# Optimization experiments

Hardware: AMD Instinct MI355X
Metric: run time of the kernel (lower is better)

The kernel has to match this reference:

```python
import jax, jax.numpy as jnp
import numpy as np

EPS = 1e-8
NUM_ITER = 3
NUM_SLOTS = 8
NUM_HEADS = 4


def _ln(x, w, b):
    m = x.mean(-1, keepdims=True)
    v = x.var(-1, keepdims=True)
    return (x - m) / jnp.sqrt(v + 1e-5) * w + b


def setup_inputs() -> dict:
    key = jax.random.key(0)
    B, T, N, D, S, H = 16, 12, 1024, 256, 128, 256
    K = NUM_SLOTS
    ks = jax.random.split(key, 32)
    w = lambda i, shape: (0.02 * jax.random.normal(ks[i], shape)).astype(jnp.float32)
    f32 = jnp.float32
    return {
        'inputs': jax.random.normal(ks[0], (B, T, N, D), f32),
        'slots_noise': jax.random.normal(ks[1], (B, K, S), f32),
        'slot_mu': w(2, (1, 1, S)),
        'slot_log_sigma': w(3, (1, 1, S)),
        'ln_in_w': jnp.ones((D,), f32), 'ln_in_b': jnp.zeros((D,), f32),
        'ln_slots_w': jnp.ones((S,), f32), 'ln_slots_b': jnp.zeros((S,), f32),
        'ln_mlp_w': jnp.ones((S,), f32), 'ln_mlp_b': jnp.zeros((S,), f32),
        'Wq': w(4, (S, S)), 'Wk': w(5, (D, S)), 'Wv': w(6, (D, S)),
        'gru_Wih': w(7, (3 * S, S)), 'gru_Whh': w(8, (3 * S, S)),
        'gru_bih': jnp.zeros((3 * S,), f32), 'gru_bhh': jnp.zeros((3 * S,), f32),
        'mlp_W1': w(9, (S, H)), 'mlp_b1': jnp.zeros((H,), f32),
        'mlp_W2': w(10, (H, S)), 'mlp_b2': jnp.zeros((S,), f32),
        'p_ln1_w': jnp.ones((S,), f32), 'p_ln1_b': jnp.zeros((S,), f32),
        'p_Wq': w(11, (S, S)), 'p_Wk': w(12, (S, S)), 'p_Wv': w(13, (S, S)), 'p_Wo': w(14, (S, S)),
        'p_ln2_w': jnp.ones((S,), f32), 'p_ln2_b': jnp.zeros((S,), f32),
        'p_ffn_W1': w(15, (S, 4 * S)), 'p_ffn_b1': jnp.zeros((4 * S,), f32),
        'p_ffn_W2': w(16, (4 * S, S)), 'p_ffn_b2': jnp.zeros((S,), f32),
        'p_lnf_w': jnp.ones((S,), f32), 'p_lnf_b': jnp.zeros((S,), f32),
    }


def reference(inputs, slots_noise, slot_mu, slot_log_sigma,
              ln_in_w, ln_in_b, ln_slots_w, ln_slots_b, ln_mlp_w, ln_mlp_b,
              Wq, Wk, Wv, gru_Wih, gru_Whh, gru_bih, gru_bhh,
              mlp_W1, mlp_b1, mlp_W2, mlp_b2,
              p_ln1_w, p_ln1_b, p_Wq, p_Wk, p_Wv, p_Wo,
              p_ln2_w, p_ln2_b, p_ffn_W1, p_ffn_b1, p_ffn_W2, p_ffn_b2,
              p_lnf_w, p_lnf_b):
    B, T, N, D = inputs.shape
    S = slot_mu.shape[-1]
    K = NUM_SLOTS

    slots0 = slot_mu + jnp.exp(slot_log_sigma) * slots_noise  # (B,K,S)
    x = _ln(inputs, ln_in_w, ln_in_b)
    k = (x @ Wk) * (S ** -0.5)  # (B,T,N,S), pre-scaled keys
    v = x @ Wv                  # (B,T,N,S)

    def gru(u, h):  # torch GRUCell semantics; u,h: (B*K,S)
        gi = u @ gru_Wih.T + gru_bih
        gh = h @ gru_Whh.T + gru_bhh
        i_r, i_z, i_n = jnp.split(gi, 3, -1)
        h_r, h_z, h_n = jnp.split(gh, 3, -1)
        r = jax.nn.sigmoid(i_r + h_r)
        z = jax.nn.sigmoid(i_z + h_z)
        n = jnp.tanh(i_n + r * h_n)
        return (1.0 - z) * n + z * h

    def mha(y):  # (B,K,S) self-attention, pre-LN block style
        dh = S // NUM_HEADS
        split = lambda t: t.reshape(B, K, NUM_HEADS, dh).transpose(0, 2, 1, 3)
        q = split(y @ p_Wq) * (dh ** -0.5)
        kk = split(y @ p_Wk)
        vv = split(y @ p_Wv)
        a = jax.nn.softmax(jnp.einsum('bhqd,bhkd->bhqk', q, kk), -1)
        o = jnp.einsum('bhqk,bhkd->bhqd', a, vv).transpose(0, 2, 1, 3).reshape(B, K, S)
        return o @ p_Wo

    def predictor(s):
        s = s + mha(_ln(s, p_ln1_w, p_ln1_b))
        h = _ln(s, p_ln2_w, p_ln2_b)
        s = s + (jax.nn.relu(h @ p_ffn_W1 + p_ffn_b1) @ p_ffn_W2 + p_ffn_b2)
        return _ln(s, p_lnf_w, p_lnf_b)

    def step(slots, kv_t):
        k_t, v_t = kv_t  # (B,N,S) each
        attn_vis = None
        for i in range(NUM_ITER):
            slots_prev = slots
            q = _ln(slots, ln_slots_w, ln_slots_b) @ Wq          # (B,K,S)
            logits = jnp.einsum('bns,bks->bnk', k_t, q)           # (B,N,K)
            attn_vis = jax.nn.softmax(logits, -1)                 # over slots
            attn = attn_vis + EPS
            attn = attn / attn.sum(1, keepdims=True)              # normalize over inputs
            updates = jnp.einsum('bnk,bns->bks', attn, v_t)       # (B,K,S)
            slots = gru(updates.reshape(-1, S), slots_prev.reshape(-1, S)).reshape(B, K, S)
            if i < NUM_ITER - 1:
                h = _ln(slots, ln_mlp_w, ln_mlp_b)
                slots = slots + (jax.nn.relu(h @ mlp_W1 + mlp_b1) @ mlp_W2 + mlp_b2)
        return predictor(slots), (slots, attn_vis)

    kT = jnp.swapaxes(k, 0, 1)  # (T,B,N,S)
    vT = jnp.swapaxes(v, 0, 1)
    _, (slots_seq, attn_seq) = jax.lax.scan(step, slots0, (kT, vT))
    slots_collect = jnp.swapaxes(slots_seq, 0, 1)  # (B,T,K,S)
    attns_collect = jnp.swapaxes(attn_seq, 0, 1)   # (B,T,N,K)
    return slots_collect, attns_collect
```

## Files before the change

### kernel.cpp

```cpp
#include <hip/hip_runtime.h>
#include <hip/hip_bf16.h>

typedef _Float16 half8 __attribute__((ext_vector_type(8)));
typedef float floatx4 __attribute__((ext_vector_type(4)));

#define MFMA_F16(a, b, c) __builtin_amdgcn_mfma_f32_16x16x32_f16((a), (b), (c), 0, 0, 0)

__global__ void prep_w_kernel(const float* __restrict__ src, _Float16* __restrict__ dst,
                              int In, int Out, float scale, int doT) {
  int idx = blockIdx.x * 256 + threadIdx.x;
  if (idx >= In * Out) return;
  float v;
  if (doT) { int o = idx / In, i = idx - o * In; v = src[i * Out + o]; }
  else     { v = src[idx]; }
  dst[idx] = (_Float16)(v * scale);
}

__global__ void init_ctr_kernel(int* __restrict__ ctr) {
  if (threadIdx.x < 16) ctr[threadIdx.x] = 0;
}

__global__ __launch_bounds__(256) void gemm_kv_kernel(
    const float* __restrict__ x, const float* __restrict__ lnw_g,
    const float* __restrict__ lnb_g, const _Float16* __restrict__ WT,
    _Float16* __restrict__ kout, _Float16* __restrict__ vTout) {
  __shared__ union {
    struct { _Float16 A[128][72]; _Float16 B[128][72]; } s;
    _Float16 C[128][136];
  } u;
  __shared__ float s_mean[128], s_rstd[128], s_red[256][2], s_lnw[256], s_lnb[256];

  const int tid = threadIdx.x;
  const int bx = blockIdx.x, y = blockIdx.y;
  const size_t r0 = (size_t)bx * 128;
  const int w = tid >> 6, lane = tid & 63, quad = lane >> 4, l15 = lane & 15;

  s_lnw[tid] = lnw_g[tid];
  s_lnb[tid] = lnb_g[tid];
  {
    int row = tid >> 1, half = tid & 1;
    const float* p = x + (r0 + row) * 256 + half * 128;
    float s = 0.f, sq = 0.f;
    for (int i = 0; i < 32; i++) {
      float4 d = ((const float4*)p)[i];
      s += d.x + d.y + d.z + d.w;
      sq += d.x * d.x + d.y * d.y + d.z * d.z + d.w * d.w;
    }
    s_red[tid][0] = s; s_red[tid][1] = sq;
  }
  __syncthreads();
  if (tid < 128) {
    float s  = s_red[2 * tid][0] + s_red[2 * tid + 1][0];
    float sq = s_red[2 * tid][1] + s_red[2 * tid + 1][1];
    float m = s * (1.f / 256.f);
    float v = sq * (1.f / 256.f) - m * m;
    s_mean[tid] = m; s_rstd[tid] = rsqrtf(v + 1e-5f);
  }

  floatx4 acc[2][8];
  for (int rt = 0; rt < 2; rt++)
    for (int ct = 0; ct < 8; ct++) acc[rt][ct] = (floatx4){0.f, 0.f, 0.f, 0.f};

  for (int c = 0; c < 4; c++) {
    __syncthreads();
    for (int i = 0; i < 4; i++) {
      int g = tid + 256 * i;
      int row = g >> 3, c8 = g & 7;
      int col0 = c * 64 + c8 * 8;
      const float* p = x + (r0 + row) * 256 + col0;
      float4 d0 = ((const float4*)p)[0];
      float4 d1 = ((const float4*)p)[1];
      float f[8] = {d0.x, d0.y, d0.z, d0.w, d1.x, d1.y, d1.z, d1.w};
      float m = s_mean[row], rs = s_rstd[row];
      half8 hv;
      #pragma unroll
      for (int j = 0; j < 8; j++)
        hv[j] = (_Float16)((f[j] - m) * rs * s_lnw[col0 + j] + s_lnb[col0 + j]);
      *(half8*)&u.s.A[row][c8 * 8] = hv;
      *(half8*)&u.s.B[row][c8 * 8] = *(const half8*)(WT + (size_t)(y * 128 + row) * 256 + col0);
    }
    __syncthreads();
    #pragma unroll
    for (int ks = 0; ks < 2; ks++) {
      half8 af[2];
      af[0] = *(const half8*)&u.s.A[(2 * w) * 16 + l15][ks * 32 + quad * 8];
      af[1] = *(const half8*)&u.s.A[(2 * w + 1) * 16 + l15][ks * 32 + quad * 8];
      #pragma unroll
      for (int ct = 0; ct < 8; ct++) {
        half8 bf = *(const half8*)&u.s.B[ct * 16 + l15][ks * 32 + quad * 8];
        acc[0][ct] = MFMA_F16(af[0], bf, acc[0][ct]);
        acc[1][ct] = MFMA_F16(af[1], bf, acc[1][ct]);
      }
    }
  }

  const size_t bt = (size_t)(bx >> 3);
  const int n0loc = (bx & 7) * 128;
  if (y == 0) {
    for (int rt = 0; rt < 2; rt++)
      for (int ct = 0; ct < 8; ct++)
        #pragma unroll
        for (int r = 0; r < 4; r++) {
          size_t row = r0 + (2 * w + rt) * 16 + quad * 4 + r;
          kout[row * 128 + ct * 16 + l15] = (_Float16)acc[rt][ct][r];
        }
  } else {
    __syncthreads();
    for (int rt = 0; rt < 2; rt++)
      for (int ct = 0; ct < 8; ct++)
        #pragma unroll
        for (int r = 0; r < 4; r++)
          u.C[(2 * w + rt) * 16 + quad * 4 + r][ct * 16 + l15] = (_Float16)acc[rt][ct][r];
    __syncthreads();
    int s = tid >> 1, hf = tid & 1;
    for (int j = 0; j < 8; j++) {
      int nb = hf * 64 + j * 8;
      half8 tmp;
      #pragma unroll
      for (int e = 0; e < 8; e++) tmp[e] = u.C[nb + e][s];
      *(half8*)(vTout + (bt * 128 + s) * 1024 + n0loc + nb) = tmp;
    }
  }
}

struct P2Args {
  const _Float16 *kbuf, *vT;
  const _Float16 *WqT, *Wih, *Whh, *W1T, *W2T;
  const _Float16 *pQT, *pKT, *pVT, *pOT, *pF1T, *pF2T;
  const float *noise, *mu, *lsig;
  const float *lnsw, *lnsb, *lnmw, *lnmb;
  const float *bih, *bhh, *mb1, *mb2;
  const float *pl1w, *pl1b, *pl2w, *pl2b, *fb1, *fb2, *plfw, *plfb;
  float *out_slots, *out_attn;
  float *upd_p;
  float *col_p;
  float *vs_p;
  int   *ctr;
};

struct SH {
  _Float16 k_lds[128][136];
  _Float16 v_lds[128][136];
  float slots[8][128];
  _Float16 a16[16][136];
  _Float16 h16[16][136];
  union {
    struct { _Float16 qT[16][136]; _Float16 attnT[16][136]; } sa;
    struct { float gi[8][384]; float gh[8][384]; } gru;
    struct { _Float16 m16[16][264]; } mlp;
    struct { float qh[8][128]; float kh[8][128]; float vh[8][128]; float sc[4][8][8]; } mha;
    struct { _Float16 f16[16][520]; } ffn;
  } u;
  float colsum[8];
  float vsum[128];
  float bih[384], bhh[384], mb1[256], mb2[128], fb1[512], fb2[128];
  float lnsw[128], lnsb[128], lnmw[128], lnmb[128];
  float pl1w[128], pl1b[128], pl2w[128], pl2b[128], plfw[128], plfb[128];
};

__device__ __forceinline__ void group_barrier(int* ctr, int target) {
  __syncthreads();
  if (threadIdx.x == 0) {
    __hip_atomic_fetch_add(ctr, 1, __ATOMIC_ACQ_REL, __HIP_MEMORY_SCOPE_AGENT);
    while (__hip_atomic_load(ctr, __ATOMIC_ACQUIRE, __HIP_MEMORY_SCOPE_AGENT) < target)
      __builtin_amdgcn_s_sleep(1);
  }
  __syncthreads();
}

__device__ __forceinline__ void ln_to_a16(SH* sh, const float (*src)[128],
                                          const float* wv, const float* bv,
                                          int w, int lane) {
  if (w < 8) {
    float x0 = src[w][lane], x1 = src[w][lane + 64];
    float s = x0 + x1, sq = x0 * x0 + x1 * x1;
    #pragma unroll
    for (int m = 1; m < 64; m <<= 1) { s += __shfl_xor(s, m); sq += __shfl_xor(sq, m); }
    float mn = s * 0.0078125f;
    float vr = sq * 0.0078125f - mn * mn;
    float rs = rsqrtf(vr + 1e-5f);
    sh->a16[w][lane]      = (_Float16)((x0 - mn) * rs * wv[lane]      + bv[lane]);
    sh->a16[w][lane + 64] = (_Float16)((x1 - mn) * rs * wv[lane + 64] + bv[lane + 64]);
  } else {
    sh->a16[w][lane] = (_Float16)0.f;
    sh->a16[w][lane + 64] = (_Float16)0.f;
  }
}

__global__ __launch_bounds__(1024) void slot_attn_kernel(P2Args P) {
  __shared__ SH sh;
  const int tid = threadIdx.x;
  const int w = tid >> 6, lane = tid & 63, quad = lane >> 4, l15 = lane & 15;
  const int b = blockIdx.x & 15;
  const int g = blockIdx.x >> 4;
  const int n0 = g * 128;
  int* ctrb = P.ctr + b;
  int bar_phase = 0;

  for (int i = tid; i < 384; i += 1024) { sh.bih[i] = P.bih[i]; sh.bhh[i] = P.bhh[i]; }
  for (int i = tid; i < 256; i += 1024) sh.mb1[i] = P.mb1[i];
  for (int i = tid; i < 512; i += 1024) sh.fb1[i] = P.fb1[i];
  if (tid < 128) {
    sh.mb2[tid]  = P.mb2[tid];  sh.fb2[tid]  = P.fb2[tid];
    sh.lnsw[tid] = P.lnsw[tid]; sh.lnsb[tid] = P.lnsb[tid];
    sh.lnmw[tid] = P.lnmw[tid]; sh.lnmb[tid] = P.lnmb[tid];
    sh.pl1w[tid] = P.pl1w[tid]; sh.pl1b[tid] = P.pl1b[tid];
    sh.pl2w[tid] = P.pl2w[tid]; sh.pl2b[tid] = P.pl2b[tid];
    sh.plfw[tid] = P.plfw[tid]; sh.plfb[tid] = P.plfb[tid];
  }
  {
    int kk = tid >> 7, s = tid & 127;
    sh.slots[kk][s] = P.mu[s] + expf(P.lsig[s]) * P.noise[(b * 8 + kk) * 128 + s];
  }
  __syncthreads();

  for (int t = 0; t < 12; t++) {
    const _Float16* kt = P.kbuf + ((size_t)(b * 12 + t)) * 1024 * 128 + (size_t)n0 * 128;
    const _Float16* vt = P.vT   + ((size_t)(b * 12 + t)) * 128 * 1024 + n0;
    {
      int r = tid >> 4, c8 = (tid & 15) * 8;
      #pragma unroll
      for (int p = 0; p < 2; p++) {
        int row = p * 64 + r;
        *(half8*)&sh.k_lds[row][c8] = *(const half8*)(kt + (size_t)row * 128 + c8);
        *(half8*)&sh.v_lds[row][c8] = *(const half8*)(vt + (size_t)row * 1024 + c8);
      }
    }
    if (tid < 128) sh.vsum[tid] = 0.f;
    __syncthreads();
    {
      int s = tid >> 3, j = tid & 7;
      float a = 0.f;
      #pragma unroll
      for (int e = 0; e < 16; e++) a += (float)sh.v_lds[s][j * 16 + e];
      atomicAdd(&sh.vsum[s], a);
    }
    __syncthreads();
    if (tid < 128)
      __hip_atomic_store(&P.vs_p[(b * 8 + g) * 128 + tid], sh.vsum[tid],
                         __ATOMIC_RELAXED, __HIP_MEMORY_SCOPE_AGENT);

    for (int it = 0; it < 3; it++) {
      const int par = (t * 3 + it) & 1;
      float* updg = P.upd_p + ((size_t)(par * 16 + b) * 8 + g) * 1024;
      float* colg = P.col_p + ((size_t)(par * 16 + b) * 8 + g) * 8;
      if (w < 8) {
        float x0 = sh.slots[w][lane], x1 = sh.slots[w][lane + 64];
        sh.h16[w][lane] = (_Float16)x0; sh.h16[w][lane + 64] = (_Float16)x1;
        float s = x0 + x1, sq = x0 * x0 + x1 * x1;
        #pragma unroll
        for (int m = 1; m < 64; m <<= 1) { s += __shfl_xor(s, m); sq += __shfl_xor(sq, m); }
        float mn = s * 0.0078125f;
        float vr = sq * 0.0078125f - mn * mn;
        float rs = rsqrtf(vr + 1e-5f);
        sh.a16[w][lane]      = (_Float16)((x0 - mn) * rs * sh.lnsw[lane]      + sh.lnsb[lane]);
        sh.a16[w][lane + 64] = (_Float16)((x1 - mn) * rs * sh.lnsw[lane + 64] + sh.lnsb[lane + 64]);
      } else {
        sh.h16[w][lane] = (_Float16)0.f; sh.h16[w][lane + 64] = (_Float16)0.f;
        sh.a16[w][lane] = (_Float16)0.f; sh.a16[w][lane + 64] = (_Float16)0.f;
      }
      if (tid < 8) sh.colsum[tid] = 0.f;
      __syncthreads();
      if (w < 8) {
        floatx4 acc = (floatx4){0.f, 0.f, 0.f, 0.f};
        const _Float16* ar = &sh.a16[l15][quad * 8];
        const _Float16* br = P.WqT + (size_t)(w * 16 + l15) * 128 + quad * 8;
        #pragma unroll
        for (int ks = 0; ks < 4; ks++)
          acc = MFMA_F16(*(const half8*)(ar + ks * 32), *(const half8*)(br + ks * 32), acc);
        #pragma unroll
        for (int r = 0; r < 4; r++)
          sh.u.sa.qT[quad * 4 + r][w * 16 + l15] = (_Float16)acc[r];
      }
      __syncthreads();
      if (w < 8) {
        int nloc0 = w * 16;
        floatx4 acc = (floatx4){0.f, 0.f, 0.f, 0.f};
        const _Float16* ar = &sh.k_lds[nloc0 + l15][quad * 8];
        const _Float16* br = &sh.u.sa.qT[l15][quad * 8];
        #pragma unroll
        for (int ks = 0; ks < 4; ks++)
          acc = MFMA_F16(*(const half8*)(ar + ks * 32), *(const half8*)(br + ks * 32), acc);
        float cs = 0.f;
        #pragma unroll
        for (int r = 0; r < 4; r++) {
          float v = (l15 < 8) ? acc[r] : -3.0e38f;
          float mx = v;
          mx = fmaxf(mx, __shfl_xor(mx, 1, 16));
          mx = fmaxf(mx, __shfl_xor(mx, 2, 16));
          mx = fmaxf(mx, __shfl_xor(mx, 4, 16));
          mx = fmaxf(mx, __shfl_xor(mx, 8, 16));
          float pv = (l15 < 8) ? expf(v - mx) : 0.f;
          float ss = pv;
          ss += __shfl_xor(ss, 1, 16); ss += __shfl_xor(ss, 2, 16);
          ss += __shfl_xor(ss, 4, 16); ss += __shfl_xor(ss, 8, 16);
          float pn = pv / ss;
          cs += pn;
          int nloc = nloc0 + quad * 4 + r;
          sh.u.sa.attnT[l15][nloc] = (_Float16)pn;
          if (it == 2 && l15 < 8)
            P.out_attn[((size_t)(b * 12 + t) * 1024 + n0 + nloc) * 8 + l15] = pn;
        }
        cs += __shfl_xor(cs, 16); cs += __shfl_xor(cs, 32);
        if (lane < 8) atomicAdd(&sh.colsum[lane], cs);
      }
      __syncthreads();
      if (w < 8) {
        floatx4 acc = (floatx4){0.f, 0.f, 0.f, 0.f};
        const _Float16* ar = &sh.u.sa.attnT[l15][quad * 8];
        const _Float16* br = &sh.v_lds[w * 16 + l15][quad * 8];
        #pragma unroll
        for (int ks = 0; ks < 4; ks++)
          acc = MFMA_F16(*(const half8*)(ar + ks * 32), *(const half8*)(br + ks * 32), acc);
        int scol = w * 16 + l15;
        #pragma unroll
        for (int r = 0; r < 4; r++) {
          int slot = quad * 4 + r;
          if (slot < 8)
            __hip_atomic_store(&updg[slot * 128 + scol], acc[r],
                               __ATOMIC_RELAXED, __HIP_MEMORY_SCOPE_AGENT);
        }
      }
      if (tid < 8)
        __hip_atomic_store(&colg[tid], sh.colsum[tid],
                           __ATOMIC_RELAXED, __HIP_MEMORY_SCOPE_AGENT);
      bar_phase++;
      group_barrier(ctrb, 8 * bar_phase);
      {
        int slot = tid >> 7, scol = tid & 127;
        const float* up = P.upd_p + (size_t)(par * 16 + b) * 8 * 1024 + slot * 128 + scol;
        float sum = 0.f;
        #pragma unroll
        for (int gg = 0; gg < 8; gg++)
          sum += __hip_atomic_load((float*)(up + gg * 1024),
                                   __ATOMIC_RELAXED, __HIP_MEMORY_SCOPE_AGENT);
        float csum = 0.f;
        if (tid < 8) {
          const float* cp = P.col_p + (size_t)(par * 16 + b) * 8 * 8 + tid;
          #pragma unroll
          for (int gg = 0; gg < 8; gg++)
            csum += __hip_atomic_load((float*)(cp + gg * 8),
                                      __ATOMIC_RELAXED, __HIP_MEMORY_SCOPE_AGENT);
        }
        float vtot = 0.f;
        if (it == 0 && tid < 128) {
          const float* vp = P.vs_p + b * 8 * 128 + tid;
          #pragma unroll
          for (int gg = 0; gg < 8; gg++)
            vtot += __hip_atomic_load((float*)(vp + gg * 128),
                                      __ATOMIC_RELAXED, __HIP_MEMORY_SCOPE_AGENT);
        }
        __syncthreads();
        if (tid < 8) sh.colsum[tid] = csum;
        if (it == 0 && tid < 128) sh.vsum[tid] = vtot;
        __syncthreads();
        float upd = (sum + 1e-8f * sh.vsum[scol]) / (sh.colsum[slot] + 1024.f * 1e-8f);
        sh.a16[slot][scol] = (_Float16)upd;
        sh.a16[slot + 8][scol] = (_Float16)0.f;
      }
      __syncthreads();
      for (int j = w; j < 48; j += 16) {
        int isGi = (j < 24) ? 1 : 0;
        int ct = isGi ? j : j - 24;
        const _Float16* Ap = isGi ? &sh.a16[0][0] : &sh.h16[0][0];
        const _Float16* Bg = (isGi ? P.Wih : P.Whh) + (size_t)(ct * 16 + l15) * 128 + quad * 8;
        const _Float16* ar = Ap + l15 * 136 + quad * 8;
        floatx4 acc = (floatx4){0.f, 0.f, 0.f, 0.f};
        #pragma unroll
        for (int ks = 0; ks < 4; ks++)
          acc = MFMA_F16(*(const half8*)(ar + ks * 32), *(const half8*)(Bg + ks * 32), acc);
        int col = ct * 16 + l15;
        float bias = isGi ? sh.bih[col] : sh.bhh[col];
        float* dst = isGi ? &sh.u.gru.gi[0][0] : &sh.u.gru.gh[0][0];
        #pragma unroll
        for (int r = 0; r < 4; r++) {
          int slot = quad * 4 + r;
          if (slot < 8) dst[slot * 384 + col] = acc[r] + bias;
        }
      }
      __syncthreads();
      {
        int kk = tid >> 7, s = tid & 127;
        float gr = sh.u.gru.gi[kk][s]       + sh.u.gru.gh[kk][s];
        float gz = sh.u.gru.gi[kk][128 + s] + sh.u.gru.gh[kk][128 + s];
        float rg = 1.f / (1.f + expf(-gr));
        float zg = 1.f / (1.f + expf(-gz));
        float ng = tanhf(sh.u.gru.gi[kk][256 + s] + rg * sh.u.gru.gh[kk][256 + s]);
        float h = sh.slots[kk][s];
        sh.slots[kk][s] = (1.f - zg) * ng + zg * h;
      }
      __syncthreads();
      if (it < 2) {
        ln_to_a16(&sh, sh.slots, sh.lnmw, sh.lnmb, w, lane);
        __syncthreads();
        {
          floatx4 acc = (floatx4){0.f, 0.f, 0.f, 0.f};
          const _Float16* ar = &sh.a16[l15][quad * 8];
          const _Float16* br = P.W1T + (size_t)(w * 16 + l15) * 128 + quad * 8;
          #pragma unroll
          for (int ks = 0; ks < 4; ks++)
            acc = MFMA_F16(*(const half8*)(ar + ks * 32), *(const half8*)(br + ks * 32), acc);
          int col = w * 16 + l15;
          #pragma unroll
          for (int r = 0; r < 4; r++) {
            int slot = quad * 4 + r;
            if (slot < 8) sh.u.mlp.m16[slot][col] = (_Float16)fmaxf(acc[r] + sh.mb1[col], 0.f);
            else          sh.u.mlp.m16[slot][col] = (_Float16)0.f;
          }
        }
        __syncthreads();
        if (w < 8) {
          floatx4 acc = (floatx4){0.f, 0.f, 0.f, 0.f};
          const _Float16* ar = &sh.u.mlp.m16[l15][quad * 8];
          const _Float16* br = P.W2T + (size_t)(w * 16 + l15) * 256 + quad * 8;
          #pragma unroll
          for (int ks = 0; ks < 8; ks++)
            acc = MFMA_F16(*(const half8*)(ar + ks * 32), *(const half8*)(br + ks * 32), acc);
          int col = w * 16 + l15;
          #pragma unroll
          for (int r = 0; r < 4; r++) {
            int slot = quad * 4 + r;
            if (slot < 8) sh.slots[slot][col] += acc[r] + sh.mb2[col];
          }
        }
        __syncthreads();
      }
    }

    if (g == 0) {
      int kk = tid >> 7, s = tid & 127;
      P.out_slots[((size_t)(b * 12 + t) * 8 + kk) * 128 + s] = sh.slots[kk][s];
    }
    ln_to_a16(&sh, sh.slots, sh.pl1w, sh.pl1b, w, lane);
    __syncthreads();
    for (int j = w; j < 24; j += 16) {
      int gg = j >> 3, ct = j & 7;
      const _Float16* Bg = (gg == 0 ? P.pQT : (gg == 1 ? P.pKT : P.pVT)) + (size_t)(ct * 16 + l15) * 128 + quad * 8;
      const _Float16* ar = &sh.a16[l15][quad * 8];
      floatx4 acc = (floatx4){0.f, 0.f, 0.f, 0.f};
      #pragma unroll
      for (int ks = 0; ks < 4; ks++)
        acc = MFMA_F16(*(const half8*)(ar + ks * 32), *(const half8*)(Bg + ks * 32), acc);
      float scale = (gg == 0) ? 0.17677669529663687f : 1.f;
      float* dst = (gg == 0 ? &sh.u.mha.qh[0][0] : (gg == 1 ? &sh.u.mha.kh[0][0] : &sh.u.mha.vh[0][0]));
      int col = ct * 16 + l15;
      #pragma unroll
      for (int r = 0; r < 4; r++) {
        int slot = quad * 4 + r;
        if (slot < 8) dst[slot * 128 + col] = acc[r] * scale;
      }
    }
    __syncthreads();
    if (tid < 256) {
      int h = tid >> 6, a = (tid >> 3) & 7, b2 = tid & 7;
      const float* qr = &sh.u.mha.qh[a][h * 32];
      const float* kr = &sh.u.mha.kh[b2][h * 32];
      float s = 0.f;
      #pragma unroll
      for (int d = 0; d < 32; d++) s += qr[d] * kr[d];
      sh.u.mha.sc[h][a][b2] = s;
    }
    __syncthreads();
    if (tid < 32) {
      int h = tid >> 3, a = tid & 7;
      float* p = sh.u.mha.sc[h][a];
      float mx = p[0];
      #pragma unroll
      for (int j = 1; j < 8; j++) mx = fmaxf(mx, p[j]);
      float e[8]; float ssum = 0.f;
      #pragma unroll
      for (int j = 0; j < 8; j++) { e[j] = expf(p[j] - mx); ssum += e[j]; }
      float inv = 1.f / ssum;
      #pragma unroll
      for (int j = 0; j < 8; j++) p[j] = e[j] * inv;
    }
    __syncthreads();
    {
      int a = tid >> 7, col = tid & 127, h = col >> 5;
      float acc = 0.f;
      #pragma unroll
      for (int b2 = 0; b2 < 8; b2++) acc += sh.u.mha.sc[h][a][b2] * sh.u.mha.vh[b2][col];
      sh.a16[a][col] = (_Float16)acc;
    }
    __syncthreads();
    if (w < 8) {
      floatx4 acc = (floatx4){0.f, 0.f, 0.f, 0.f};
      const _Float16* ar = &sh.a16[l15][quad * 8];
      const _Float16* br = P.pOT + (size_t)(w * 16 + l15) * 128 + quad * 8;
      #pragma unroll
      for (int ks = 0; ks < 4; ks++)
        acc = MFMA_F16(*(const half8*)(ar + ks * 32), *(const half8*)(br + ks * 32), acc);
      int col = w * 16 + l15;
      #pragma unroll
      for (int r = 0; r < 4; r++) {
        int slot = quad * 4 + r;
        if (slot < 8) sh.slots[slot][col] += acc[r];
      }
    }
    __syncthreads();
    ln_to_a16(&sh, sh.slots, sh.pl2w, sh.pl2b, w, lane);
    __syncthreads();
    for (int ct = w; ct < 32; ct += 16) {
      floatx4 acc = (floatx4){0.f, 0.f, 0.f, 0.f};
      const _Float16* ar = &sh.a16[l15][quad * 8];
      const _Float16* br = P.pF1T + (size_t)(ct * 16 + l15) * 128 + quad * 8;
      #pragma unroll
      for (int ks = 0; ks < 4; ks++)
        acc = MFMA_F16(*(const half8*)(ar + ks * 32), *(const half8*)(br + ks * 32), acc);
      int col = ct * 16 + l15;
      #pragma unroll
      for (int r = 0; r < 4; r++) {
        int slot = quad * 4 + r;
        if (slot < 8) sh.u.ffn.f16[slot][col] = (_Float16)fmaxf(acc[r] + sh.fb1[col], 0.f);
        else          sh.u.ffn.f16[slot][col] = (_Float16)0.f;
      }
    }
    __syncthreads();
    if (w < 8) {
      floatx4 acc = (floatx4){0.f, 0.f, 0.f, 0.f};
      const _Float16* ar = &sh.u.ffn.f16[l15][quad * 8];
      const _Float16* br = P.pF2T + (size_t)(w * 16 + l15) * 512 + quad * 8;
      #pragma unroll 4
      for (int ks = 0; ks < 16; ks++)
        acc = MFMA_F16(*(const half8*)(ar + ks * 32), *(const half8*)(br + ks * 32), acc);
      int col = w * 16 + l15;
      #pragma unroll
      for (int r = 0; r < 4; r++) {
        int slot = quad * 4 + r;
        if (slot < 8) sh.slots[slot][col] += acc[r] + sh.fb2[col];
      }
    }
    __syncthreads();
    if (w < 8) {
      float x0 = sh.slots[w][lane], x1 = sh.slots[w][lane + 64];
      float s = x0 + x1, sq = x0 * x0 + x1 * x1;
      #pragma unroll
      for (int m = 1; m < 64; m <<= 1) { s += __shfl_xor(s, m); sq += __shfl_xor(sq, m); }
      float mn = s * 0.0078125f;
      float vr = sq * 0.0078125f - mn * mn;
      float rs = rsqrtf(vr + 1e-5f);
      sh.slots[w][lane]      = (x0 - mn) * rs * sh.plfw[lane]      + sh.plfb[lane];
      sh.slots[w][lane + 64] = (x1 - mn) * rs * sh.plfw[lane + 64] + sh.plfb[lane + 64];
    }
    __syncthreads();
  }
}

extern "C" void kernel_launch(void* const* d_in, const int* in_sizes, int n_in,
                              void* d_out, int out_size, void* d_ws, size_t ws_size,
                              hipStream_t stream) {
  const float* inp   = (const float*)d_in[0];
  const float* noise = (const float*)d_in[1];
  const float* mu    = (const float*)d_in[2];
  const float* lsig  = (const float*)d_in[3];
  const float* lniw  = (const float*)d_in[4];
  const float* lnib  = (const float*)d_in[5];
  const float* lnsw  = (const float*)d_in[6];
  const float* lnsb  = (const float*)d_in[7];
  const float* lnmw  = (const float*)d_in[8];
  const float* lnmb  = (const float*)d_in[9];
  const float* Wq    = (const float*)d_in[10];
  const float* Wk    = (const float*)d_in[11];
  const float* Wv    = (const float*)d_in[12];
  const float* gWih  = (const float*)d_in[13];
  const float* gWhh  = (const float*)d_in[14];
  const float* gbih  = (const float*)d_in[15];
  const float* gbhh  = (const float*)d_in[16];
  const float* mW1   = (const float*)d_in[17];
  const float* mb1   = (const float*)d_in[18];
  const float* mW2   = (const float*)d_in[19];
  const float* mb2   = (const float*)d_in[20];
  const float* pl1w  = (const float*)d_in[21];
  const float* pl1b  = (const float*)d_in[22];
  const float* pWq   = (const float*)d_in[23];
  const float* pWk   = (const float*)d_in[24];
  const float* pWv   = (const float*)d_in[25];
  const float* pWo   = (const float*)d_in[26];
  const float* pl2w  = (const float*)d_in[27];
  const float* pl2b  = (const float*)d_in[28];
  const float* pf1   = (const float*)d_in[29];
  const float* pfb1  = (const float*)d_in[30];
  const float* pf2   = (const float*)d_in[31];
  const float* pfb2  = (const float*)d_in[32];
  const float* plfw  = (const float*)d_in[33];
  const float* plfb  = (const float*)d_in[34];

  _Float16* p   = (_Float16*)d_ws;
  _Float16* kbuf = p;  p += 25165824;
  _Float16* vT   = p;  p += 25165824;
  _Float16* WT   = p;  p += 65536;
  _Float16* WqT  = p;  p += 16384;
  _Float16* Wih  = p;  p += 49152;
  _Float16* Whh  = p;  p += 49152;
  _Float16* W1T  = p;  p += 32768;
  _Float16* W2T  = p;  p += 32768;
  _Float16* pQT  = p;  p += 16384;
  _Float16* pKT  = p;  p += 16384;
  _Float16* pVT  = p;  p += 16384;
  _Float16* pOT  = p;  p += 16384;
  _Float16* pF1T = p;  p += 65536;
  _Float16* pF2T = p;  p += 65536;
  float* fb   = (float*)p;
  float* upd_p = fb;  fb += 2 * 16 * 8 * 1024;
  float* col_p = fb;  fb += 2 * 16 * 8 * 8;
  float* vs_p  = fb;  fb += 16 * 8 * 128;
  int*   ctr   = (int*)fb;

  const float kscale = 0.08838834764831845f;
  init_ctr_kernel<<<1, 64, 0, stream>>>(ctr);
  prep_w_kernel<<<128, 256, 0, stream>>>(Wk,   WT,         256, 128, kscale, 1);
  prep_w_kernel<<<128, 256, 0, stream>>>(Wv,   WT + 32768, 256, 128, 1.f,    1);
  prep_w_kernel<<<64,  256, 0, stream>>>(Wq,   WqT,        128, 128, 1.f,    1);
  prep_w_kernel<<<192, 256, 0, stream>>>(gWih, Wih,        49152, 1, 1.f,    0);
  prep_w_kernel<<<192, 256, 0, stream>>>(gWhh, Whh,        49152, 1, 1.f,    0);
  prep_w_kernel<<<128, 256, 0, stream>>>(mW1,  W1T,        128, 256, 1.f,    1);
  prep_w_kernel<<<128, 256, 0, stream>>>(mW2,  W2T,        256, 128, 1.f,    1);
  prep_w_kernel<<<64,  256, 0, stream>>>(pWq,  pQT,        128, 128, 1.f,    1);
  prep_w_kernel<<<64,  256, 0, stream>>>(pWk,  pKT,        128, 128, 1.f,    1);
  prep_w_kernel<<<64,  256, 0, stream>>>(pWv,  pVT,        128, 128, 1.f,    1);
  prep_w_kernel<<<64,  256, 0, stream>>>(pWo,  pOT,        128, 128, 1.f,    1);
  prep_w_kernel<<<256, 256, 0, stream>>>(pf1,  pF1T,       128, 512, 1.f,    1);
  prep_w_kernel<<<256, 256, 0, stream>>>(pf2,  pF2T,       512, 128, 1.f,    1);

  dim3 g1(1536, 2, 1);
  gemm_kv_kernel<<<g1, 256, 0, stream>>>(inp, lniw, lnib, WT, kbuf, vT);

  P2Args a;
  a.kbuf = kbuf; a.vT = vT;
  a.WqT = WqT; a.Wih = Wih; a.Whh = Whh; a.W1T = W1T; a.W2T = W2T;
  a.pQT = pQT; a.pKT = pKT; a.pVT = pVT; a.pOT = pOT; a.pF1T = pF1T; a.pF2T = pF2T;
  a.noise = noise; a.mu = mu; a.lsig = lsig;
  a.lnsw = lnsw; a.lnsb = lnsb; a.lnmw = lnmw; a.lnmb = lnmb;
  a.bih = gbih; a.bhh = gbhh; a.mb1 = mb1; a.mb2 = mb2;
  a.pl1w = pl1w; a.pl1b = pl1b; a.pl2w = pl2w; a.pl2b = pl2b;
  a.fb1 = pfb1; a.fb2 = pfb2; a.plfw = plfw; a.plfb = plfb;
  a.out_slots = (float*)d_out;
  a.out_attn  = (float*)d_out + 196608;
  a.upd_p = upd_p; a.col_p = col_p; a.vs_p = vs_p; a.ctr = ctr;

  slot_attn_kernel<<<128, 1024, 0, stream>>>(a);
}
```

Baseline: 1.375 ms.

## Merge prep launches, fuse K/V GEMM into one block, split slot attention across 16 groups

All weight-prep launches and the counter init are folded into one kernel that dispatches on block index. The K/V projection now computes both K and V in a single block over a 256-wide weight tile, so the input LayerNorm and its loads happen once instead of twice. The recurrent slot-attention kernel moves from 128 blocks of 1024 threads to 256 blocks of 512 threads, each handling 64 tokens with 16 groups per batch, and removes idle half-warps. It also fuses the Wq and GRU Whh MFMAs and the predictor QKV projections into single passes. The cost is more partial sums and larger cross-block barriers per batch.

```diff
diff --git a/kernel.cpp b/kernel.cpp
--- a/kernel.cpp
+++ b/kernel.cpp
@@ -6,18 +6,25 @@
 
 #define MFMA_F16(a, b, c) __builtin_amdgcn_mfma_f32_16x16x32_f16((a), (b), (c), 0, 0, 0)
 
-__global__ void prep_w_kernel(const float* __restrict__ src, _Float16* __restrict__ dst,
-                              int In, int Out, float scale, int doT) {
-  int idx = blockIdx.x * 256 + threadIdx.x;
-  if (idx >= In * Out) return;
+struct PrepArgs {
+  const float* src[13]; _Float16* dst[13];
+  int In[13]; int On[13]; float scale[13]; int doT[13];
+  int pre[14];
+  int* ctr;
+};
+
+__global__ void prep_all_kernel(PrepArgs A) {
+  if (blockIdx.x == 0 && threadIdx.x < 16) A.ctr[threadIdx.x] = 0;
+  int j = 0;
+  #pragma unroll 1
+  while (j < 12 && (int)blockIdx.x >= A.pre[j + 1]) j++;
+  int idx = (blockIdx.x - A.pre[j]) * 256 + threadIdx.x;
+  int In = A.In[j], On = A.On[j];
+  if (idx >= In * On) return;
   float v;
-  if (doT) { int o = idx / In, i = idx - o * In; v = src[i * Out + o]; }
-  else     { v = src[idx]; }
-  dst[idx] = (_Float16)(v * scale);
-}
-
-__global__ void init_ctr_kernel(int* __restrict__ ctr) {
-  if (threadIdx.x < 16) ctr[threadIdx.x] = 0;
+  if (A.doT[j]) { int o = idx / In, i = idx - o * In; v = A.src[j][i * On + o]; }
+  else          { v = A.src[j][idx]; }
+  A.dst[j][idx] = (_Float16)(v * A.scale[j]);
 }
 
 __global__ __launch_bounds__(256) void gemm_kv_kernel(
@@ -25,13 +32,13 @@
     const float* __restrict__ lnb_g, const _Float16* __restrict__ WT,
     _Float16* __restrict__ kout, _Float16* __restrict__ vTout) {
   __shared__ union {
-    struct { _Float16 A[128][72]; _Float16 B[128][72]; } s;
+    struct { _Float16 A[128][72]; _Float16 B[256][72]; } s;
     _Float16 C[128][136];
   } u;
   __shared__ float s_mean[128], s_rstd[128], s_red[256][2], s_lnw[256], s_lnb[256];
 
   const int tid = threadIdx.x;
-  const int bx = blockIdx.x, y = blockIdx.y;
+  const int bx = blockIdx.x;
   const size_t r0 = (size_t)bx * 128;
   const int w = tid >> 6, lane = tid & 63, quad = lane >> 4, l15 = lane & 15;
 
@@ -57,15 +64,15 @@
     s_mean[tid] = m; s_rstd[tid] = rsqrtf(v + 1e-5f);
   }
 
-  floatx4 acc[2][8];
+  floatx4 acc[2][16];
   for (int rt = 0; rt < 2; rt++)
-    for (int ct = 0; ct < 8; ct++) acc[rt][ct] = (floatx4){0.f, 0.f, 0.f, 0.f};
+    for (int ct = 0; ct < 16; ct++) acc[rt][ct] = (floatx4){0.f, 0.f, 0.f, 0.f};
 
   for (int c = 0; c < 4; c++) {
     __syncthreads();
     for (int i = 0; i < 4; i++) {
-      int g = tid + 256 * i;
-      int row = g >> 3, c8 = g & 7;
+      int gg = tid + 256 * i;
+      int row = gg >> 3, c8 = gg & 7;
       int col0 = c * 64 + c8 * 8;
       const float* p = x + (r0 + row) * 256 + col0;
       float4 d0 = ((const float4*)p)[0];
@@ -77,7 +84,12 @@
       for (int j = 0; j < 8; j++)
         hv[j] = (_Float16)((f[j] - m) * rs * s_lnw[col0 + j] + s_lnb[col0 + j]);
       *(half8*)&u.s.A[row][c8 * 8] = hv;
-      *(half8*)&u.s.B[row][c8 * 8] = *(const half8*)(WT + (size_t)(y * 128 + row) * 256 + col0);
+    }
+    for (int i = 0; i < 8; i++) {
+      int gg = tid + 256 * i;
+      int row = gg >> 3, c8 = gg & 7;
+      int col0 = c * 64 + c8 * 8;
+      *(half8*)&u.s.B[row][c8 * 8] = *(const half8*)(WT + (size_t)row * 256 + col0);
     }
     __syncthreads();
     #pragma unroll
@@ -86,7 +98,7 @@
       af[0] = *(const half8*)&u.s.A[(2 * w) * 16 + l15][ks * 32 + quad * 8];
       af[1] = *(const half8*)&u.s.A[(2 * w + 1) * 16 + l15][ks * 32 + quad * 8];
       #pragma unroll
-      for (int ct = 0; ct < 8; ct++) {
+      for (int ct = 0; ct < 16; ct++) {
         half8 bf = *(const half8*)&u.s.B[ct * 16 + l15][ks * 32 + quad * 8];
         acc[0][ct] = MFMA_F16(af[0], bf, acc[0][ct]);
         acc[1][ct] = MFMA_F16(af[1], bf, acc[1][ct]);
@@ -94,32 +106,29 @@
     }
   }
 
+  for (int rt = 0; rt < 2; rt++)
+    for (int ct = 0; ct < 8; ct++)
+      #pragma unroll
+      for (int r = 0; r < 4; r++) {
+        size_t row = r0 + (2 * w + rt) * 16 + quad * 4 + r;
+        kout[row * 128 + ct * 16 + l15] = (_Float16)acc[rt][ct][r];
+      }
+  __syncthreads();
+  for (int rt = 0; rt < 2; rt++)
+    for (int ct = 8; ct < 16; ct++)
+      #pragma unroll
+      for (int r = 0; r < 4; r++)
+        u.C[(2 * w + rt) * 16 + quad * 4 + r][(ct - 8) * 16 + l15] = (_Float16)acc[rt][ct][r];
+  __syncthreads();
   const size_t bt = (size_t)(bx >> 3);
   const int n0loc = (bx & 7) * 128;
-  if (y == 0) {
-    for (int rt = 0; rt < 2; rt++)
-      for (int ct = 0; ct < 8; ct++)
-        #pragma unroll
-        for (int r = 0; r < 4; r++) {
-          size_t row = r0 + (2 * w + rt) * 16 + quad * 4 + r;
-          kout[row * 128 + ct * 16 + l15] = (_Float16)acc[rt][ct][r];
-        }
-  } else {
-    __syncthreads();
-    for (int rt = 0; rt < 2; rt++)
-      for (int ct = 0; ct < 8; ct++)
-        #pragma unroll
-        for (int r = 0; r < 4; r++)
-          u.C[(2 * w + rt) * 16 + quad * 4 + r][ct * 16 + l15] = (_Float16)acc[rt][ct][r];
-    __syncthreads();
-    int s = tid >> 1, hf = tid & 1;
-    for (int j = 0; j < 8; j++) {
-      int nb = hf * 64 + j * 8;
-      half8 tmp;
-      #pragma unroll
-      for (int e = 0; e < 8; e++) tmp[e] = u.C[nb + e][s];
-      *(half8*)(vTout + (bt * 128 + s) * 1024 + n0loc + nb) = tmp;
-    }
+  int s = tid >> 1, hf = tid & 1;
+  for (int j = 0; j < 8; j++) {
+    int nb = hf * 64 + j * 8;
+    half8 tmp;
+    #pragma unroll
+    for (int e = 0; e < 8; e++) tmp[e] = u.C[nb + e][s];
+    *(half8*)(vTout + (bt * 128 + s) * 1024 + n0loc + nb) = tmp;
   }
 }
 
@@ -139,14 +148,13 @@
 };
 
 struct SH {
-  _Float16 k_lds[128][136];
-  _Float16 v_lds[128][136];
+  _Float16 k_lds[64][136];
+  _Float16 v_lds[128][72];
   float slots[8][128];
   _Float16 a16[16][136];
   _Float16 h16[16][136];
   union {
-    struct { _Float16 qT[16][136]; _Float16 attnT[16][136]; } sa;
-    struct { float gi[8][384]; float gh[8][384]; } gru;
+    struct { _Float16 qT[16][136]; _Float16 attnT[16][72]; } sa;
     struct { _Float16 m16[16][264]; } mlp;
     struct { float qh[8][128]; float kh[8][128]; float vh[8][128]; float sc[4][8][8]; } mha;
     struct { _Float16 f16[16][520]; } ffn;
@@ -168,38 +176,32 @@
   __syncthreads();
 }
 
-__device__ __forceinline__ void ln_to_a16(SH* sh, const float (*src)[128],
-                                          const float* wv, const float* bv,
+__device__ __forceinline__ void ln_to_a16(SH* sh, const float* wv, const float* bv,
                                           int w, int lane) {
-  if (w < 8) {
-    float x0 = src[w][lane], x1 = src[w][lane + 64];
-    float s = x0 + x1, sq = x0 * x0 + x1 * x1;
-    #pragma unroll
-    for (int m = 1; m < 64; m <<= 1) { s += __shfl_xor(s, m); sq += __shfl_xor(sq, m); }
-    float mn = s * 0.0078125f;
-    float vr = sq * 0.0078125f - mn * mn;
-    float rs = rsqrtf(vr + 1e-5f);
-    sh->a16[w][lane]      = (_Float16)((x0 - mn) * rs * wv[lane]      + bv[lane]);
-    sh->a16[w][lane + 64] = (_Float16)((x1 - mn) * rs * wv[lane + 64] + bv[lane + 64]);
-  } else {
-    sh->a16[w][lane] = (_Float16)0.f;
-    sh->a16[w][lane + 64] = (_Float16)0.f;
-  }
+  float x0 = sh->slots[w][lane], x1 = sh->slots[w][lane + 64];
+  float s = x0 + x1, sq = x0 * x0 + x1 * x1;
+  #pragma unroll
+  for (int m = 1; m < 64; m <<= 1) { s += __shfl_xor(s, m); sq += __shfl_xor(sq, m); }
+  float mn = s * 0.0078125f;
+  float vr = sq * 0.0078125f - mn * mn;
+  float rs = rsqrtf(vr + 1e-5f);
+  sh->a16[w][lane]      = (_Float16)((x0 - mn) * rs * wv[lane]      + bv[lane]);
+  sh->a16[w][lane + 64] = (_Float16)((x1 - mn) * rs * wv[lane + 64] + bv[lane + 64]);
 }
 
-__global__ __launch_bounds__(1024) void slot_attn_kernel(P2Args P) {
+__global__ __launch_bounds__(512) void slot_attn_kernel(P2Args P) {
   __shared__ SH sh;
   const int tid = threadIdx.x;
   const int w = tid >> 6, lane = tid & 63, quad = lane >> 4, l15 = lane & 15;
   const int b = blockIdx.x & 15;
   const int g = blockIdx.x >> 4;
-  const int n0 = g * 128;
+  const int n0 = g * 64;
   int* ctrb = P.ctr + b;
   int bar_phase = 0;
 
-  for (int i = tid; i < 384; i += 1024) { sh.bih[i] = P.bih[i]; sh.bhh[i] = P.bhh[i]; }
-  for (int i = tid; i < 256; i += 1024) sh.mb1[i] = P.mb1[i];
-  for (int i = tid; i < 512; i += 1024) sh.fb1[i] = P.fb1[i];
+  for (int i = tid; i < 384; i += 512) { sh.bih[i] = P.bih[i]; sh.bhh[i] = P.bhh[i]; }
+  if (tid < 256) sh.mb1[tid] = P.mb1[tid];
+  sh.fb1[tid] = P.fb1[tid];
   if (tid < 128) {
     sh.mb2[tid]  = P.mb2[tid];  sh.fb2[tid]  = P.fb2[tid];
     sh.lnsw[tid] = P.lnsw[tid]; sh.lnsb[tid] = P.lnsb[tid];
@@ -208,43 +210,59 @@
     sh.pl2w[tid] = P.pl2w[tid]; sh.pl2b[tid] = P.pl2b[tid];
     sh.plfw[tid] = P.plfw[tid]; sh.plfb[tid] = P.plfb[tid];
   }
+  for (int i = tid; i < 1024; i += 512) {
+    int kk = i >> 7, s = i & 127;
+    sh.slots[kk][s] = P.mu[s] + expf(P.lsig[s]) * P.noise[(b * 8 + kk) * 128 + s];
+  }
   {
-    int kk = tid >> 7, s = tid & 127;
-    sh.slots[kk][s] = P.mu[s] + expf(P.lsig[s]) * P.noise[(b * 8 + kk) * 128 + s];
+    _Float16* pa = &sh.a16[8][0];
+    _Float16* ph = &sh.h16[8][0];
+    for (int i = tid; i < 8 * 136; i += 512) { pa[i] = (_Float16)0.f; ph[i] = (_Float16)0.f; }
   }
   __syncthreads();
 
   for (int t = 0; t < 12; t++) {
     const _Float16* kt = P.kbuf + ((size_t)(b * 12 + t)) * 1024 * 128 + (size_t)n0 * 128;
     const _Float16* vt = P.vT   + ((size_t)(b * 12 + t)) * 128 * 1024 + n0;
+    for (int e = tid; e < 1024; e += 512) {
+      int row = e >> 4, c8 = (e & 15) * 8;
+      *(half8*)&sh.k_lds[row][c8] = *(const half8*)(kt + (size_t)row * 128 + c8);
+    }
+    for (int e = tid; e < 1024; e += 512) {
+      int row = e >> 3, c8 = (e & 7) * 8;
+      *(half8*)&sh.v_lds[row][c8] = *(const half8*)(vt + (size_t)row * 1024 + c8);
+    }
+    if (tid < 128) sh.vsum[tid] = 0.f;
+    if (tid < 8) sh.colsum[tid] = 0.f;
+    __syncthreads();
     {
-      int r = tid >> 4, c8 = (tid & 15) * 8;
-      #pragma unroll
-      for (int p = 0; p < 2; p++) {
-        int row = p * 64 + r;
-        *(half8*)&sh.k_lds[row][c8] = *(const half8*)(kt + (size_t)row * 128 + c8);
-        *(half8*)&sh.v_lds[row][c8] = *(const half8*)(vt + (size_t)row * 1024 + c8);
-      }
-    }
-    if (tid < 128) sh.vsum[tid] = 0.f;
-    __syncthreads();
+      int s = tid >> 2, j = tid & 3;
+      half8 h0 = *(const half8*)&sh.v_lds[s][j * 16];
+      half8 h1 = *(const half8*)&sh.v_lds[s][j * 16 + 8];
+      float a = 0.f;
+      #pragma unroll
+      for (int e = 0; e < 8; e++) a += (float)h0[e] + (float)h1[e];
+      atomicAdd(&sh.vsum[s], a);
+    }
     {
-      int s = tid >> 3, j = tid & 7;
-      float a = 0.f;
-      #pragma unroll
-      for (int e = 0; e < 16; e++) a += (float)sh.v_lds[s][j * 16 + e];
-      atomicAdd(&sh.vsum[s], a);
-    }
-    __syncthreads();
-    if (tid < 128)
-      __hip_atomic_store(&P.vs_p[(b * 8 + g) * 128 + tid], sh.vsum[tid],
-                         __ATOMIC_RELAXED, __HIP_MEMORY_SCOPE_AGENT);
+      float x0 = sh.slots[w][lane], x1 = sh.slots[w][lane + 64];
+      sh.h16[w][lane] = (_Float16)x0; sh.h16[w][lane + 64] = (_Float16)x1;
+      float s = x0 + x1, sq = x0 * x0 + x1 * x1;
+      #pragma unroll
+      for (int m = 1; m < 64; m <<= 1) { s += __shfl_xor(s, m); sq += __shfl_xor(sq, m); }
+      float mn = s * 0.0078125f;
+      float vr = sq * 0.0078125f - mn * mn;
+      float rs = rsqrtf(vr + 1e-5f);
+      sh.a16[w][lane]      = (_Float16)((x0 - mn) * rs * sh.lnsw[lane]      + sh.lnsb[lane]);
+      sh.a16[w][lane + 64] = (_Float16)((x1 - mn) * rs * sh.lnsw[lane + 64] + sh.lnsb[lane + 64]);
+    }
+    __syncthreads();
 
     for (int it = 0; it < 3; it++) {
       const int par = (t * 3 + it) & 1;
-      float* updg = P.upd_p + ((size_t)(par * 16 + b) * 8 + g) * 1024;
-      float* colg = P.col_p + ((size_t)(par * 16 + b) * 8 + g) * 8;
-      if (w < 8) {
+      float* updg = P.upd_p + ((size_t)(par * 16 + b) * 16 + g) * 1024;
+      float* colg = P.col_p + ((size_t)(par * 16 + b) * 16 + g) * 8;
+      if (it > 0) {
         float x0 = sh.slots[w][lane], x1 = sh.slots[w][lane + 64];
         sh.h16[w][lane] = (_Float16)x0; sh.h16[w][lane + 64] = (_Float16)x1;
         float s = x0 + x1, sq = x0 * x0 + x1 * x1;
@@ -255,27 +273,37 @@
         float rs = rsqrtf(vr + 1e-5f);
         sh.a16[w][lane]      = (_Float16)((x0 - mn) * rs * sh.lnsw[lane]      + sh.lnsb[lane]);
         sh.a16[w][lane + 64] = (_Float16)((x1 - mn) * rs * sh.lnsw[lane + 64] + sh.lnsb[lane + 64]);
-      } else {
-        sh.h16[w][lane] = (_Float16)0.f; sh.h16[w][lane + 64] = (_Float16)0.f;
-        sh.a16[w][lane] = (_Float16)0.f; sh.a16[w][lane + 64] = (_Float16)0.f;
-      }
-      if (tid < 8) sh.colsum[tid] = 0.f;
+        if (tid < 8) sh.colsum[tid] = 0.f;
+        __syncthreads();
+      }
+      floatx4 ghr = (floatx4){0.f,0.f,0.f,0.f}, ghz = ghr, ghn = ghr;
+      {
+        floatx4 aq = (floatx4){0.f,0.f,0.f,0.f};
+        const _Float16* ar = &sh.a16[l15][quad * 8];
+        const _Float16* hr = &sh.h16[l15][quad * 8];
+        const _Float16* bq = P.WqT + (size_t)(w * 16 + l15) * 128 + quad * 8;
+        const _Float16* br_ = P.Whh + (size_t)(w * 16 + l15) * 128 + quad * 8;
+        const _Float16* bz = P.Whh + (size_t)((w + 8) * 16 + l15) * 128 + quad * 8;
+        const _Float16* bn = P.Whh + (size_t)((w + 16) * 16 + l15) * 128 + quad * 8;
+        #pragma unroll
+        for (int ks = 0; ks < 4; ks++) {
+          half8 hf = *(const half8*)(hr + ks * 32);
+          aq  = MFMA_F16(*(const half8*)(ar + ks * 32), *(const half8*)(bq + ks * 32), aq);
+          ghr = MFMA_F16(hf, *(const half8*)(br_ + ks * 32), ghr);
+          ghz = MFMA_F16(hf, *(const half8*)(bz + ks * 32), ghz);
+          ghn = MFMA_F16(hf, *(const half8*)(bn + ks * 32), ghn);
+        }
+        #pragma unroll
+        for (int r = 0; r < 4; r++)
+          sh.u.sa.qT[quad * 4 + r][w * 16 + l15] = (_Float16)aq[r];
+      }
+      if (it == 0 && tid < 128)
+        __hip_atomic_store(&P.vs_p[(b * 16 + g) * 128 + tid], sh.vsum[tid],
+                           __ATOMIC_RELAXED, __HIP_MEMORY_SCOPE_AGENT);
       __syncthreads();
-      if (w < 8) {
-        floatx4 acc = (floatx4){0.f, 0.f, 0.f, 0.f};
-        const _Float16* ar = &sh.a16[l15][quad * 8];
-        const _Float16* br = P.WqT + (size_t)(w * 16 + l15) * 128 + quad * 8;
-        #pragma unroll
-        for (int ks = 0; ks < 4; ks++)
-          acc = MFMA_F16(*(const half8*)(ar + ks * 32), *(const half8*)(br + ks * 32), acc);
-        #pragma unroll
-        for (int r = 0; r < 4; r++)
-          sh.u.sa.qT[quad * 4 + r][w * 16 + l15] = (_Float16)acc[r];
-      }
-      __syncthreads();
-      if (w < 8) {
+      if (w < 4) {
         int nloc0 = w * 16;
-        floatx4 acc = (floatx4){0.f, 0.f, 0.f, 0.f};
+        floatx4 acc = (floatx4){0.f,0.f,0.f,0.f};
         const _Float16* ar = &sh.k_lds[nloc0 + l15][quad * 8];
         const _Float16* br = &sh.u.sa.qT[l15][quad * 8];
         #pragma unroll
@@ -305,19 +333,18 @@
         if (lane < 8) atomicAdd(&sh.colsum[lane], cs);
       }
       __syncthreads();
-      if (w < 8) {
-        floatx4 acc = (floatx4){0.f, 0.f, 0.f, 0.f};
+      {
+        floatx4 acc = (floatx4){0.f,0.f,0.f,0.f};
         const _Float16* ar = &sh.u.sa.attnT[l15][quad * 8];
         const _Float16* br = &sh.v_lds[w * 16 + l15][quad * 8];
         #pragma unroll
-        for (int ks = 0; ks < 4; ks++)
+        for (int ks = 0; ks < 2; ks++)
           acc = MFMA_F16(*(const half8*)(ar + ks * 32), *(const half8*)(br + ks * 32), acc);
         int scol = w * 16 + l15;
-        #pragma unroll
-        for (int r = 0; r < 4; r++) {
-          int slot = quad * 4 + r;
-          if (slot < 8)
-            __hip_atomic_store(&updg[slot * 128 + scol], acc[r],
+        if (quad < 2) {
+          #pragma unroll
+          for (int r = 0; r < 4; r++)
+            __hip_atomic_store(&updg[(quad * 4 + r) * 128 + scol], acc[r],
                                __ATOMIC_RELAXED, __HIP_MEMORY_SCOPE_AGENT);
         }
       }
@@ -325,102 +352,112 @@
         __hip_atomic_store(&colg[tid], sh.colsum[tid],
                            __ATOMIC_RELAXED, __HIP_MEMORY_SCOPE_AGENT);
       bar_phase++;
-      group_barrier(ctrb, 8 * bar_phase);
+      group_barrier(ctrb, 16 * bar_phase);
       {
-        int slot = tid >> 7, scol = tid & 127;
-        const float* up = P.upd_p + (size_t)(par * 16 + b) * 8 * 1024 + slot * 128 + scol;
-        float sum = 0.f;
-        #pragma unroll
-        for (int gg = 0; gg < 8; gg++)
-          sum += __hip_atomic_load((float*)(up + gg * 1024),
+        float sum[2];
+        #pragma unroll
+        for (int p = 0; p < 2; p++) {
+          int i = tid + p * 512;
+          int slot = i >> 7, scol = i & 127;
+          const float* up = P.upd_p + (size_t)(par * 16 + b) * 16 * 1024 + slot * 128 + scol;
+          float s = 0.f;
+          #pragma unroll
+          for (int gg = 0; gg < 16; gg++)
+            s += __hip_atomic_load((float*)(up + gg * 1024),
                                    __ATOMIC_RELAXED, __HIP_MEMORY_SCOPE_AGENT);
+          sum[p] = s;
+        }
         float csum = 0.f;
         if (tid < 8) {
-          const float* cp = P.col_p + (size_t)(par * 16 + b) * 8 * 8 + tid;
-          #pragma unroll
-          for (int gg = 0; gg < 8; gg++)
+          const float* cp = P.col_p + (size_t)(par * 16 + b) * 16 * 8 + tid;
+          #pragma unroll
+          for (int gg = 0; gg < 16; gg++)
             csum += __hip_atomic_load((float*)(cp + gg * 8),
                                       __ATOMIC_RELAXED, __HIP_MEMORY_SCOPE_AGENT);
         }
         float vtot = 0.f;
         if (it == 0 && tid < 128) {
-          const float* vp = P.vs_p + b * 8 * 128 + tid;
-          #pragma unroll
-          for (int gg = 0; gg < 8; gg++)
+          const float* vp = P.vs_p + b * 16 * 128 + tid;
+          #pragma unroll
+          for (int gg = 0; gg < 16; gg++)
             vtot += __hip_atomic_load((float*)(vp + gg * 128),
                                       __ATOMIC_RELAXED, __HIP_MEMORY_SCOPE_AGENT);
         }
-        __syncthreads();
         if (tid < 8) sh.colsum[tid] = csum;
         if (it == 0 && tid < 128) sh.vsum[tid] = vtot;
         __syncthreads();
-        float upd = (sum + 1e-8f * sh.vsum[scol]) / (sh.colsum[slot] + 1024.f * 1e-8f);
-        sh.a16[slot][scol] = (_Float16)upd;
-        sh.a16[slot + 8][scol] = (_Float16)0.f;
-      }
-      __syncthreads();
-      for (int j = w; j < 48; j += 16) {
-        int isGi = (j < 24) ? 1 : 0;
-        int ct = isGi ? j : j - 24;
-        const _Float16* Ap = isGi ? &sh.a16[0][0] : &sh.h16[0][0];
-        const _Float16* Bg = (isGi ? P.Wih : P.Whh) + (size_t)(ct * 16 + l15) * 128 + quad * 8;
-        const _Float16* ar = Ap + l15 * 136 + quad * 8;
-        floatx4 acc = (floatx4){0.f, 0.f, 0.f, 0.f};
-        #pragma unroll
-        for (int ks = 0; ks < 4; ks++)
-          acc = MFMA_F16(*(const half8*)(ar + ks * 32), *(const half8*)(Bg + ks * 32), acc);
-        int col = ct * 16 + l15;
-        float bias = isGi ? sh.bih[col] : sh.bhh[col];
-        float* dst = isGi ? &sh.u.gru.gi[0][0] : &sh.u.gru.gh[0][0];
-        #pragma unroll
-        for (int r = 0; r < 4; r++) {
-          int slot = quad * 4 + r;
-          if (slot < 8) dst[slot * 384 + col] = acc[r] + bias;
+        #pragma unroll
+        for (int p = 0; p < 2; p++) {
+          int i = tid + p * 512;
+          int slot = i >> 7, scol = i & 127;
+          float upd = (sum[p] + 1e-8f * sh.vsum[scol]) / (sh.colsum[slot] + 1024.f * 1e-8f);
+          sh.a16[slot][scol] = (_Float16)upd;
         }
       }
       __syncthreads();
       {
-        int kk = tid >> 7, s = tid & 127;
-        float gr = sh.u.gru.gi[kk][s]       + sh.u.gru.gh[kk][s];
-        float gz = sh.u.gru.gi[kk][128 + s] + sh.u.gru.gh[kk][128 + s];
-        float rg = 1.f / (1.f + expf(-gr));
-        float zg = 1.f / (1.f + expf(-gz));
-        float ng = tanhf(sh.u.gru.gi[kk][256 + s] + rg * sh.u.gru.gh[kk][256 + s]);
-        float h = sh.slots[kk][s];
-        sh.slots[kk][s] = (1.f - zg) * ng + zg * h;
+        floatx4 gir = (floatx4){0.f,0.f,0.f,0.f}, giz = gir, gin = gir;
+        const _Float16* ar = &sh.a16[l15][quad * 8];
+        const _Float16* br_ = P.Wih + (size_t)(w * 16 + l15) * 128 + quad * 8;
+        const _Float16* bz = P.Wih + (size_t)((w + 8) * 16 + l15) * 128 + quad * 8;
+        const _Float16* bn = P.Wih + (size_t)((w + 16) * 16 + l15) * 128 + quad * 8;
+        #pragma unroll
+        for (int ks = 0; ks < 4; ks++) {
+          half8 af = *(const half8*)(ar + ks * 32);
+          gir = MFMA_F16(af, *(const half8*)(br_ + ks * 32), gir);
+          giz = MFMA_F16(af, *(const half8*)(bz + ks * 32), giz);
+          gin = MFMA_F16(af, *(const half8*)(bn + ks * 32), gin);
+        }
+        int c = w * 16 + l15;
+        if (quad < 2) {
+          float b_r = sh.bih[c],       h_r = sh.bhh[c];
+          float b_z = sh.bih[128 + c], h_z = sh.bhh[128 + c];
+          float b_n = sh.bih[256 + c], h_n = sh.bhh[256 + c];
+          #pragma unroll
+          for (int r = 0; r < 4; r++) {
+            int slot = quad * 4 + r;
+            float grv = gir[r] + b_r + ghr[r] + h_r;
+            float gzv = giz[r] + b_z + ghz[r] + h_z;
+            float rg = 1.f / (1.f + expf(-grv));
+            float zg = 1.f / (1.f + expf(-gzv));
+            float ng = tanhf(gin[r] + b_n + rg * (ghn[r] + h_n));
+            float h = sh.slots[slot][c];
+            sh.slots[slot][c] = (1.f - zg) * ng + zg * h;
+          }
+        }
       }
       __syncthreads();
       if (it < 2) {
-        ln_to_a16(&sh, sh.slots, sh.lnmw, sh.lnmb, w, lane);
+        ln_to_a16(&sh, sh.lnmw, sh.lnmb, w, lane);
+        __syncthreads();
+        for (int ct = w; ct < 16; ct += 8) {
+          floatx4 acc = (floatx4){0.f,0.f,0.f,0.f};
+          const _Float16* ar = &sh.a16[l15][quad * 8];
+          const _Float16* br = P.W1T + (size_t)(ct * 16 + l15) * 128 + quad * 8;
+          #pragma unroll
+          for (int ks = 0; ks < 4; ks++)
+            acc = MFMA_F16(*(const half8*)(ar + ks * 32), *(const half8*)(br + ks * 32), acc);
+          int col = ct * 16 + l15;
+          #pragma unroll
+          for (int r = 0; r < 4; r++) {
+            int slot = quad * 4 + r;
+            sh.u.mlp.m16[slot][col] = (slot < 8) ? (_Float16)fmaxf(acc[r] + sh.mb1[col], 0.f)
+                                                 : (_Float16)0.f;
+          }
+        }
         __syncthreads();
         {
-          floatx4 acc = (floatx4){0.f, 0.f, 0.f, 0.f};
-          const _Float16* ar = &sh.a16[l15][quad * 8];
-          const _Float16* br = P.W1T + (size_t)(w * 16 + l15) * 128 + quad * 8;
-          #pragma unroll
-          for (int ks = 0; ks < 4; ks++)
-            acc = MFMA_F16(*(const half8*)(ar + ks * 32), *(const half8*)(br + ks * 32), acc);
-          int col = w * 16 + l15;
-          #pragma unroll
-          for (int r = 0; r < 4; r++) {
-            int slot = quad * 4 + r;
-            if (slot < 8) sh.u.mlp.m16[slot][col] = (_Float16)fmaxf(acc[r] + sh.mb1[col], 0.f);
-            else          sh.u.mlp.m16[slot][col] = (_Float16)0.f;
-          }
-        }
-        __syncthreads();
-        if (w < 8) {
-          floatx4 acc = (floatx4){0.f, 0.f, 0.f, 0.f};
+          floatx4 acc = (floatx4){0.f,0.f,0.f,0.f};
           const _Float16* ar = &sh.u.mlp.m16[l15][quad * 8];
           const _Float16* br = P.W2T + (size_t)(w * 16 + l15) * 256 + quad * 8;
           #pragma unroll
           for (int ks = 0; ks < 8; ks++)
             acc = MFMA_F16(*(const half8*)(ar + ks * 32), *(const half8*)(br + ks * 32), acc);
           int col = w * 16 + l15;
-          #pragma unroll
-          for (int r = 0; r < 4; r++) {
-            int slot = quad * 4 + r;
-            if (slot < 8) sh.slots[slot][col] += acc[r] + sh.mb2[col];
+          if (quad < 2) {
+            #pragma unroll
+            for (int r = 0; r < 4; r++)
+              sh.slots[quad * 4 + r][col] += acc[r] + sh.mb2[col];
           }
         }
         __syncthreads();
@@ -428,26 +465,35 @@
     }
 
     if (g == 0) {
-      int kk = tid >> 7, s = tid & 127;
-      P.out_slots[((size_t)(b * 12 + t) * 8 + kk) * 128 + s] = sh.slots[kk][s];
-    }
-    ln_to_a16(&sh, sh.slots, sh.pl1w, sh.pl1b, w, lane);
-    __syncthreads();
-    for (int j = w; j < 24; j += 16) {
-      int gg = j >> 3, ct = j & 7;
-      const _Float16* Bg = (gg == 0 ? P.pQT : (gg == 1 ? P.pKT : P.pVT)) + (size_t)(ct * 16 + l15) * 128 + quad * 8;
+      for (int i = tid; i < 1024; i += 512) {
+        int kk = i >> 7, s = i & 127;
+        P.out_slots[((size_t)(b * 12 + t) * 8 + kk) * 128 + s] = sh.slots[kk][s];
+      }
+    }
+    ln_to_a16(&sh, sh.pl1w, sh.pl1b, w, lane);
+    __syncthreads();
+    {
+      floatx4 aq = (floatx4){0.f,0.f,0.f,0.f}, ak = aq, av = aq;
       const _Float16* ar = &sh.a16[l15][quad * 8];
-      floatx4 acc = (floatx4){0.f, 0.f, 0.f, 0.f};
-      #pragma unroll
-      for (int ks = 0; ks < 4; ks++)
-        acc = MFMA_F16(*(const half8*)(ar + ks * 32), *(const half8*)(Bg + ks * 32), acc);
-      float scale = (gg == 0) ? 0.17677669529663687f : 1.f;
-      float* dst = (gg == 0 ? &sh.u.mha.qh[0][0] : (gg == 1 ? &sh.u.mha.kh[0][0] : &sh.u.mha.vh[0][0]));
-      int col = ct * 16 + l15;
-      #pragma unroll
-      for (int r = 0; r < 4; r++) {
-        int slot = quad * 4 + r;
-        if (slot < 8) dst[slot * 128 + col] = acc[r] * scale;
+      const _Float16* bq = P.pQT + (size_t)(w * 16 + l15) * 128 + quad * 8;
+      const _Float16* bk = P.pKT + (size_t)(w * 16 + l15) * 128 + quad * 8;
+      const _Float16* bv = P.pVT + (size_t)(w * 16 + l15) * 128 + quad * 8;
+      #pragma unroll
+      for (int ks = 0; ks < 4; ks++) {
+        half8 af = *(const half8*)(ar + ks * 32);
+        aq = MFMA_F16(af, *(const half8*)(bq + ks * 32), aq);
+        ak = MFMA_F16(af, *(const half8*)(bk + ks * 32), ak);
+        av = MFMA_F16(af, *(const half8*)(bv + ks * 32), av);
+      }
+      int col = w * 16 + l15;
+      if (quad < 2) {
+        #pragma unroll
+        for (int r = 0; r < 4; r++) {
+          int slot = quad * 4 + r;
+          sh.u.mha.qh[slot][col] = aq[r] * 0.17677669529663687f;
+          sh.u.mha.kh[slot][col] = ak[r];
+          sh.u.mha.vh[slot][col] = av[r];
+        }
       }
     }
     __syncthreads();
@@ -475,33 +521,33 @@
       for (int j = 0; j < 8; j++) p[j] = e[j] * inv;
     }
     __syncthreads();
-    {
-      int a = tid >> 7, col = tid & 127, h = col >> 5;
+    for (int i = tid; i < 1024; i += 512) {
+      int a = i >> 7, col = i & 127, h = col >> 5;
       float acc = 0.f;
       #pragma unroll
       for (int b2 = 0; b2 < 8; b2++) acc += sh.u.mha.sc[h][a][b2] * sh.u.mha.vh[b2][col];
       sh.a16[a][col] = (_Float16)acc;
     }
     __syncthreads();
-    if (w < 8) {
-      floatx4 acc = (floatx4){0.f, 0.f, 0.f, 0.f};
+    {
+      floatx4 acc = (floatx4){0.f,0.f,0.f,0.f};
       const _Float16* ar = &sh.a16[l15][quad * 8];
       const _Float16* br = P.pOT + (size_t)(w * 16 + l15) * 128 + quad * 8;
       #pragma unroll
       for (int ks = 0; ks < 4; ks++)
         acc = MFMA_F16(*(const half8*)(ar + ks * 32), *(const half8*)(br + ks * 32), acc);
       int col = w * 16 + l15;
-      #pragma unroll
-      for (int r = 0; r < 4; r++) {
-        int slot = quad * 4 + r;
-        if (slot < 8) sh.slots[slot][col] += acc[r];
-      }
-    }
-    __syncthreads();
-    ln_to_a16(&sh, sh.slots, sh.pl2w, sh.pl2b, w, lane);
-    __syncthreads();
-    for (int ct = w; ct < 32; ct += 16) {
-      floatx4 acc = (floatx4){0.f, 0.f, 0.f, 0.f};
+      if (quad < 2) {
+        #pragma unroll
+        for (int r = 0; r < 4; r++)
+          sh.slots[quad * 4 + r][col] += acc[r];
+      }
+    }
+    __syncthreads();
+    ln_to_a16(&sh, sh.pl2w, sh.pl2b, w, lane);
+    __syncthreads();
+    for (int ct = w; ct < 32; ct += 8) {
+      floatx4 acc = (floatx4){0.f,0.f,0.f,0.f};
       const _Float16* ar = &sh.a16[l15][quad * 8];
       const _Float16* br = P.pF1T + (size_t)(ct * 16 + l15) * 128 + quad * 8;
       #pragma unroll
@@ -511,27 +557,27 @@
       #pragma unroll
       for (int r = 0; r < 4; r++) {
         int slot = quad * 4 + r;
-        if (slot < 8) sh.u.ffn.f16[slot][col] = (_Float16)fmaxf(acc[r] + sh.fb1[col], 0.f);
-        else          sh.u.ffn.f16[slot][col] = (_Float16)0.f;
-      }
-    }
-    __syncthreads();
-    if (w < 8) {
-      floatx4 acc = (floatx4){0.f, 0.f, 0.f, 0.f};
+        sh.u.ffn.f16[slot][col] = (slot < 8) ? (_Float16)fmaxf(acc[r] + sh.fb1[col], 0.f)
+                                             : (_Float16)0.f;
+      }
+    }
+    __syncthreads();
+    {
+      floatx4 acc = (floatx4){0.f,0.f,0.f,0.f};
       const _Float16* ar = &sh.u.ffn.f16[l15][quad * 8];
       const _Float16* br = P.pF2T + (size_t)(w * 16 + l15) * 512 + quad * 8;
       #pragma unroll 4
       for (int ks = 0; ks < 16; ks++)
         acc = MFMA_F16(*(const half8*)(ar + ks * 32), *(const half8*)(br + ks * 32), acc);
       int col = w * 16 + l15;
-      #pragma unroll
-      for (int r = 0; r < 4; r++) {
-        int slot = quad * 4 + r;
-        if (slot < 8) sh.slots[slot][col] += acc[r] + sh.fb2[col];
-      }
-    }
-    __syncthreads();
-    if (w < 8) {
+      if (quad < 2) {
+        #pragma unroll
+        for (int r = 0; r < 4; r++)
+          sh.slots[quad * 4 + r][col] += acc[r] + sh.fb2[col];
+      }
+    }
+    __syncthreads();
+    {
       float x0 = sh.slots[w][lane], x1 = sh.slots[w][lane + 64];
       float s = x0 + x1, sq = x0 * x0 + x1 * x1;
       #pragma unroll
@@ -601,29 +647,32 @@
   _Float16* pF1T = p;  p += 65536;
   _Float16* pF2T = p;  p += 65536;
   float* fb   = (float*)p;
-  float* upd_p = fb;  fb += 2 * 16 * 8 * 1024;
-  float* col_p = fb;  fb += 2 * 16 * 8 * 8;
-  float* vs_p  = fb;  fb += 16 * 8 * 128;
+  float* upd_p = fb;  fb += 2 * 16 * 16 * 1024;
+  float* col_p = fb;  fb += 2 * 16 * 16 * 8;
+  float* vs_p  = fb;  fb += 16 * 16 * 128;
   int*   ctr   = (int*)fb;
 
   const float kscale = 0.08838834764831845f;
-  init_ctr_kernel<<<1, 64, 0, stream>>>(ctr);
-  prep_w_kernel<<<128, 256, 0, stream>>>(Wk,   WT,         256, 128, kscale, 1);
-  prep_w_kernel<<<128, 256, 0, stream>>>(Wv,   WT + 32768, 256, 128, 1.f,    1);
-  prep_w_kernel<<<64,  256, 0, stream>>>(Wq,   WqT,        128, 128, 1.f,    1);
-  prep_w_kernel<<<192, 256, 0, stream>>>(gWih, Wih,        49152, 1, 1.f,    0);
-  prep_w_kernel<<<192, 256, 0, stream>>>(gWhh, Whh,        49152, 1, 1.f,    0);
-  prep_w_kernel<<<128, 256, 0, stream>>>(mW1,  W1T,        128, 256, 1.f,    1);
-  prep_w_kernel<<<128, 256, 0, stream>>>(mW2,  W2T,        256, 128, 1.f,    1);
-  prep_w_kernel<<<64,  256, 0, stream>>>(pWq,  pQT,        128, 128, 1.f,    1);
-  prep_w_kernel<<<64,  256, 0, stream>>>(pWk,  pKT,        128, 128, 1.f,    1);
-  prep_w_kernel<<<64,  256, 0, stream>>>(pWv,  pVT,        128, 128, 1.f,    1);
-  prep_w_kernel<<<64,  256, 0, stream>>>(pWo,  pOT,        128, 128, 1.f,    1);
-  prep_w_kernel<<<256, 256, 0, stream>>>(pf1,  pF1T,       128, 512, 1.f,    1);
-  prep_w_kernel<<<256, 256, 0, stream>>>(pf2,  pF2T,       512, 128, 1.f,    1);
-
-  dim3 g1(1536, 2, 1);
-  gemm_kv_kernel<<<g1, 256, 0, stream>>>(inp, lniw, lnib, WT, kbuf, vT);
+
+  PrepArgs pa;
+  const float* srcs[13] = {Wk, Wv, Wq, gWih, gWhh, mW1, mW2, pWq, pWk, pWv, pWo, pf1, pf2};
+  _Float16* dsts[13] = {WT, WT + 32768, WqT, Wih, Whh, W1T, W2T, pQT, pKT, pVT, pOT, pF1T, pF2T};
+  int Ins[13]  = {256, 256, 128, 49152, 49152, 128, 256, 128, 128, 128, 128, 128, 512};
+  int Ons[13]  = {128, 128, 128, 1,     1,     256, 128, 128, 128, 128, 128, 512, 128};
+  float scs[13] = {kscale, 1.f, 1.f, 1.f, 1.f, 1.f, 1.f, 1.f, 1.f, 1.f, 1.f, 1.f, 1.f};
+  int dts[13]  = {1, 1, 1, 0, 0, 1, 1, 1, 1, 1, 1, 1, 1};
+  int total = 0;
+  for (int j = 0; j < 13; j++) {
+    pa.src[j] = srcs[j]; pa.dst[j] = dsts[j];
+    pa.In[j] = Ins[j]; pa.On[j] = Ons[j]; pa.scale[j] = scs[j]; pa.doT[j] = dts[j];
+    pa.pre[j] = total;
+    total += (Ins[j] * Ons[j] + 255) / 256;
+  }
+  pa.pre[13] = total;
+  pa.ctr = ctr;
+  prep_all_kernel<<<total, 256, 0, stream>>>(pa);
+
+  gemm_kv_kernel<<<1536, 256, 0, stream>>>(inp, lniw, lnib, WT, kbuf, vT);
 
   P2Args a;
   a.kbuf = kbuf; a.vT = vT;
@@ -638,5 +687,5 @@
   a.out_attn  = (float*)d_out + 196608;
   a.upd_p = upd_p; a.col_p = col_p; a.vs_p = vs_p; a.ctr = ctr;
 
-  slot_attn_kernel<<<128, 1024, 0, stream>>>(a);
+  slot_attn_kernel<<<256, 512, 0, stream>>>(a);
 }
```

Result: slower. 1.414 ms (+2.8%).
